# Optimization experiments

Hardware: AMD Instinct MI355X
Metric: run time of the kernel (lower is better)

Reference implementation:

```python
import jax, jax.numpy as jnp
import numpy as np

D_MODEL = 1024
DK = 64
N_HEADS = D_MODEL // DK
MASK = True


def setup_inputs() -> dict:
    key = jax.random.key(0)
    ks = jax.random.split(key, 8)
    B, S = 4, 2048
    scale = 1.0 / np.sqrt(D_MODEL)
    return {
        "query_data": jax.random.normal(ks[0], (B, S, D_MODEL), dtype=jnp.float32),
        "key_data": jax.random.normal(ks[1], (B, S, D_MODEL), dtype=jnp.float32),
        "value_data": jax.random.normal(ks[2], (B, S, D_MODEL), dtype=jnp.float32),
        "Wq": jax.random.normal(ks[3], (D_MODEL, D_MODEL), dtype=jnp.float32) * scale,
        "Wk": jax.random.normal(ks[4], (D_MODEL, D_MODEL), dtype=jnp.float32) * scale,
        "Wv": jax.random.normal(ks[5], (D_MODEL, D_MODEL), dtype=jnp.float32) * scale,
        "Wp": jax.random.normal(ks[6], (D_MODEL, D_MODEL), dtype=jnp.float32) * scale,
        "bp": jnp.zeros((D_MODEL,), dtype=jnp.float32),
    }


def reference(query_data, key_data, value_data, Wq, Wk, Wv, Wp, bp):
    B, S, _ = query_data.shape
    # QKV projections, split into heads: (B, H, S, dk)
    def split_heads(x, W):
        return (x @ W.T).reshape(B, -1, N_HEADS, DK).transpose(0, 2, 1, 3)

    q = split_heads(query_data, Wq)
    k = split_heads(key_data, Wk)
    v = split_heads(value_data, Wv)

    scores = jnp.einsum("bhqd,bhkd->bhqk", q, k) / np.sqrt(DK).astype(np.float32)
    if MASK:
        Sq, Sk = scores.shape[-2], scores.shape[-1]
        causal = jnp.triu(jnp.ones((Sq, Sk), dtype=scores.dtype), k=1) * jnp.float32(-1e13)
        scores = scores + causal  # broadcast over (B, H)
    attn = jax.nn.softmax(scores, axis=-1)
    out = jnp.einsum("bhqk,bhkd->bhqd", attn, v)
    out = out.transpose(0, 2, 1, 3).reshape(B, S, D_MODEL)
    # dropout is identity in eval mode
    return out @ Wp.T + bp
```

## Files before the change

### kernel.cpp

```cpp
#include <hip/hip_runtime.h>
#include <stdint.h>

#define D_MODEL 1024
#define SEQ     2048
#define BATCH   4
#define NH      16
#define DKK     64
#define MROWS   (BATCH * SEQ)

typedef unsigned short u16;
using bf16x8 = __attribute__((ext_vector_type(8))) __bf16;
using f32x4  = __attribute__((ext_vector_type(4))) float;

__device__ __forceinline__ u16 f2bf(float f) {
    union { float f; uint32_t u; } v; v.f = f;
    return (u16)((v.u + 0x7FFFu + ((v.u >> 16) & 1u)) >> 16);
}

__device__ __forceinline__ float fast_exp2(float x) {
    float r; asm("v_exp_f32 %0, %1" : "=v"(r) : "v"(x)); return r;
}
__device__ __forceinline__ float fast_rcp(float x) {
    float r; asm("v_rcp_f32 %0, %1" : "=v"(r) : "v"(x)); return r;
}

__device__ __forceinline__ void gl_lds16(const u16* g, u16* l) {
    __builtin_amdgcn_global_load_lds(
        (__attribute__((address_space(1))) void*)(const_cast<u16*>(g)),
        (__attribute__((address_space(3))) void*)l, 16, 0, 0);
}

__global__ __launch_bounds__(256) void cvt3_kernel(const float* __restrict__ a,
                                                   const float* __restrict__ b,
                                                   const float* __restrict__ c,
                                                   u16* __restrict__ da,
                                                   u16* __restrict__ db,
                                                   u16* __restrict__ dc) {
    const int i = blockIdx.x * 256 + threadIdx.x;
    const int sel = i >> 21, off = i & ((1 << 21) - 1);
    const float* s = (sel == 0) ? a : (sel == 1) ? b : c;
    u16* d = (sel == 0) ? da : (sel == 1) ? db : dc;
    float4 v = ((const float4*)s)[off];
    ushort4 o;
    o.x = f2bf(v.x); o.y = f2bf(v.y); o.z = f2bf(v.z); o.w = f2bf(v.w);
    ((ushort4*)d)[off] = o;
}

__global__ __launch_bounds__(256) void cvt4_kernel(const float* __restrict__ a,
                                                   const float* __restrict__ b,
                                                   const float* __restrict__ c,
                                                   const float* __restrict__ d4,
                                                   u16* __restrict__ da,
                                                   u16* __restrict__ db,
                                                   u16* __restrict__ dc,
                                                   u16* __restrict__ dd) {
    const int i = blockIdx.x * 256 + threadIdx.x;
    const int sel = i >> 18, off = i & ((1 << 18) - 1);
    const float* s = (sel == 0) ? a : (sel == 1) ? b : (sel == 2) ? c : d4;
    u16* d = (sel == 0) ? da : (sel == 1) ? db : (sel == 2) ? dc : dd;
    float4 v = ((const float4*)s)[off];
    ushort4 o;
    o.x = f2bf(v.x); o.y = f2bf(v.y); o.z = f2bf(v.z); o.w = f2bf(v.w);
    ((ushort4*)d)[off] = o;
}

__global__ __launch_bounds__(256, 2) void gemm_qkv(const u16* __restrict__ XQ,
                                                   const u16* __restrict__ XK,
                                                   const u16* __restrict__ XV,
                                                   const u16* __restrict__ WQ,
                                                   const u16* __restrict__ WK,
                                                   const u16* __restrict__ WV,
                                                   u16* __restrict__ Qo,
                                                   u16* __restrict__ Ko,
                                                   u16* __restrict__ Vto) {
    constexpr int K = 1024, N = 1024;
    __shared__ u16 ldsA[128 * 32];
    __shared__ u16 ldsB[128 * 32];

    const int which = blockIdx.x >> 9;
    const int inner = blockIdx.x & 511;
    const u16* A  = (which == 0) ? XQ : (which == 1) ? XK : XV;
    const u16* Bw = (which == 0) ? WQ : (which == 1) ? WK : WV;

    const int t = threadIdx.x;
    const int w = t >> 6, lane = t & 63;
    const int quad = lane >> 4, l15 = lane & 15;
    const int bn = inner & 7, bm = inner >> 3;
    const int wm = (w >> 1) * 64, wn = (w & 1) * 64;

    const u16* Ab = A  + (size_t)bm * 128 * K;
    const u16* Bb = Bw + (size_t)bn * 128 * K;
    const int srow  = lane >> 2;
    const int scol8 = (lane & 3) * 8;

    f32x4 acc[4][4];
    #pragma unroll
    for (int i = 0; i < 4; ++i)
        #pragma unroll
        for (int j = 0; j < 4; ++j)
            acc[i][j] = f32x4{0.f, 0.f, 0.f, 0.f};

    for (int k0 = 0; k0 < K; k0 += 32) {
        __syncthreads();
        #pragma unroll
        for (int i = 0; i < 2; ++i) {
            const int c = w * 2 + i;
            gl_lds16(Ab + (size_t)(c * 16 + srow) * K + k0 + scol8, &ldsA[c * 512]);
            gl_lds16(Bb + (size_t)(c * 16 + srow) * K + k0 + scol8, &ldsB[c * 512]);
        }
        __syncthreads();

        bf16x8 afr[4], bfr[4];
        #pragma unroll
        for (int i = 0; i < 4; ++i)
            afr[i] = *(const bf16x8*)&ldsA[(wm + i * 16 + l15) * 32 + quad * 8];
        #pragma unroll
        for (int j = 0; j < 4; ++j)
            bfr[j] = *(const bf16x8*)&ldsB[(wn + j * 16 + l15) * 32 + quad * 8];

        #pragma unroll
        for (int i = 0; i < 4; ++i)
            #pragma unroll
            for (int j = 0; j < 4; ++j)
                acc[i][j] = __builtin_amdgcn_mfma_f32_16x16x32_bf16(afr[i], bfr[j], acc[i][j], 0, 0, 0);
    }

    if (which < 2) {
        u16* outb = which ? Ko : Qo;
        #pragma unroll
        for (int i = 0; i < 4; ++i)
            #pragma unroll
            for (int j = 0; j < 4; ++j)
                #pragma unroll
                for (int r = 0; r < 4; ++r) {
                    const int row = bm * 128 + wm + i * 16 + quad * 4 + r;
                    const int col = bn * 128 + wn + j * 16 + l15;
                    outb[(size_t)row * N + col] = f2bf(acc[i][j][r]);
                }
    } else {
        #pragma unroll
        for (int i = 0; i < 4; ++i)
            #pragma unroll
            for (int j = 0; j < 4; ++j)
                #pragma unroll
                for (int r = 0; r < 4; ++r) {
                    const int row = bm * 128 + wm + i * 16 + quad * 4 + r;
                    const int col = bn * 128 + wn + j * 16 + l15;
                    const int bb = row >> 11, ss = row & 2047;
                    const int hh = col >> 6,  dd = col & 63;
                    Vto[(size_t)((bb * NH + hh) * DKK + dd) * SEQ + ss] = f2bf(acc[i][j][r]);
                }
    }
}

__global__ __launch_bounds__(256, 2) void gemm_proj(const u16* __restrict__ A,
                                                    const u16* __restrict__ Bw,
                                                    float* __restrict__ outf,
                                                    const float* __restrict__ bias) {
    constexpr int K = 1024, N = 1024;
    __shared__ u16 ldsA[128 * 32];
    __shared__ u16 ldsB[128 * 32];

    const int t = threadIdx.x;
    const int w = t >> 6, lane = t & 63;
    const int quad = lane >> 4, l15 = lane & 15;
    const int bn = blockIdx.x & 7, bm = blockIdx.x >> 3;
    const int wm = (w >> 1) * 64, wn = (w & 1) * 64;

    const u16* Ab = A  + (size_t)bm * 128 * K;
    const u16* Bb = Bw + (size_t)bn * 128 * K;
    const int srow  = lane >> 2;
    const int scol8 = (lane & 3) * 8;

    f32x4 acc[4][4];
    #pragma unroll
    for (int i = 0; i < 4; ++i)
        #pragma unroll
        for (int j = 0; j < 4; ++j)
            acc[i][j] = f32x4{0.f, 0.f, 0.f, 0.f};

    for (int k0 = 0; k0 < K; k0 += 32) {
        __syncthreads();
        #pragma unroll
        for (int i = 0; i < 2; ++i) {
            const int c = w * 2 + i;
            gl_lds16(Ab + (size_t)(c * 16 + srow) * K + k0 + scol8, &ldsA[c * 512]);
            gl_lds16(Bb + (size_t)(c * 16 + srow) * K + k0 + scol8, &ldsB[c * 512]);
        }
        __syncthreads();

        bf16x8 afr[4], bfr[4];
        #pragma unroll
        for (int i = 0; i < 4; ++i)
            afr[i] = *(const bf16x8*)&ldsA[(wm + i * 16 + l15) * 32 + quad * 8];
        #pragma unroll
        for (int j = 0; j < 4; ++j)
            bfr[j] = *(const bf16x8*)&ldsB[(wn + j * 16 + l15) * 32 + quad * 8];

        #pragma unroll
        for (int i = 0; i < 4; ++i)
            #pragma unroll
            for (int j = 0; j < 4; ++j)
                acc[i][j] = __builtin_amdgcn_mfma_f32_16x16x32_bf16(afr[i], bfr[j], acc[i][j], 0, 0, 0);
    }

    #pragma unroll
    for (int i = 0; i < 4; ++i)
        #pragma unroll
        for (int j = 0; j < 4; ++j)
            #pragma unroll
            for (int r = 0; r < 4; ++r) {
                const int row = bm * 128 + wm + i * 16 + quad * 4 + r;
                const int col = bn * 128 + wn + j * 16 + l15;
                outf[(size_t)row * N + col] = acc[i][j][r] + bias[col];
            }
}

__global__ __launch_bounds__(256, 4) void flash_attn(const u16* __restrict__ Qb,
                                                     const u16* __restrict__ Kb,
                                                     const u16* __restrict__ Vt,
                                                     u16* __restrict__ O) {
    __shared__ u16 ldsK[2 * 4096];
    __shared__ u16 ldsV[2 * 4096];
    __shared__ u16 ldsP[4 * 1024];

    const int t = threadIdx.x;
    const int w = t >> 6, lane = t & 63;
    const int quad = lane >> 4, l15 = lane & 15;
    const int bh = blockIdx.x & 63;
    const int qt = blockIdx.x >> 6;
    const int b = bh >> 4, h = bh & 15;
    const int q0 = qt * 64;
    const int qw = q0 + w * 16;

    const int srow  = lane >> 2;
    const int scol8 = (lane & 3) * 8;
    const size_t kbase = (size_t)b * SEQ * D_MODEL + h * DKK;
    const size_t vbase = (size_t)(bh * DKK) * SEQ;

    const u16* Qrow = Qb + (size_t)(b * SEQ + qw + l15) * D_MODEL + h * DKK;
    const bf16x8 qf0 = *(const bf16x8*)(Qrow + quad * 8);
    const bf16x8 qf1 = *(const bf16x8*)(Qrow + 32 + quad * 8);

    bf16x8 onesf;
    {
        union { bf16x8 v; u16 s[8]; } uu;
        const u16 ov = (l15 == 0) ? (u16)0x3F80 : (u16)0;
        #pragma unroll
        for (int j = 0; j < 8; ++j) uu.s[j] = ov;
        onesf = uu.v;
    }

    f32x4 o_acc[4];
    #pragma unroll
    for (int nt = 0; nt < 4; ++nt) o_acc[nt] = f32x4{0.f, 0.f, 0.f, 0.f};
    float m_i[4], l_i[4];
    #pragma unroll
    for (int r = 0; r < 4; ++r) { m_i[r] = -1e30f; l_i[r] = 0.f; }

    const float C2 = 0.18033688f;

    {
        #pragma unroll
        for (int i = 0; i < 2; ++i) {
            const int e = w * 2 + i, ch = e >> 2, rb = (e & 3) * 16;
            gl_lds16(Kb + kbase + (size_t)(0 + rb + srow) * D_MODEL + ch * 32 + scol8,
                     &ldsK[ch * 2048 + rb * 32]);
            gl_lds16(Vt + vbase + (size_t)(rb + srow) * SEQ + 0 + ch * 32 + scol8,
                     &ldsV[ch * 2048 + rb * 32]);
        }
    }

    int cur = 0;
    for (int it = 0; it <= qt; ++it) {
        const int kb = it * 64;
        __syncthreads();

        if (it < qt) {
            const int nb = (it + 1) * 64, nxt = cur ^ 1;
            #pragma unroll
            for (int i = 0; i < 2; ++i) {
                const int e = w * 2 + i, ch = e >> 2, rb = (e & 3) * 16;
                gl_lds16(Kb + kbase + (size_t)(nb + rb + srow) * D_MODEL + ch * 32 + scol8,
                         &ldsK[nxt * 4096 + ch * 2048 + rb * 32]);
                gl_lds16(Vt + vbase + (size_t)(rb + srow) * SEQ + nb + ch * 32 + scol8,
                         &ldsV[nxt * 4096 + ch * 2048 + rb * 32]);
            }
        }

        f32x4 sc[4];
        #pragma unroll
        for (int jt = 0; jt < 4; ++jt) sc[jt] = f32x4{0.f, 0.f, 0.f, 0.f};
        #pragma unroll
        for (int ks = 0; ks < 2; ++ks) {
            const bf16x8 qf = ks ? qf1 : qf0;
            #pragma unroll
            for (int jt = 0; jt < 4; ++jt) {
                bf16x8 kf = *(const bf16x8*)&ldsK[cur * 4096 + ks * 2048 + (jt * 16 + l15) * 32 + quad * 8];
                sc[jt] = __builtin_amdgcn_mfma_f32_16x16x32_bf16(qf, kf, sc[jt], 0, 0, 0);
            }
        }

        if (kb + 63 > qw) {
            #pragma unroll
            for (int jt = 0; jt < 4; ++jt)
                #pragma unroll
                for (int r = 0; r < 4; ++r)
                    if (kb + jt * 16 + l15 > qw + quad * 4 + r) sc[jt][r] = -3.0e38f;
        }

        float tmax[4];
        #pragma unroll
        for (int r = 0; r < 4; ++r)
            tmax[r] = fmaxf(fmaxf(sc[0][r], sc[1][r]), fmaxf(sc[2][r], sc[3][r]));
        #pragma unroll
        for (int off = 1; off < 16; off <<= 1)
            #pragma unroll
            for (int r = 0; r < 4; ++r)
                tmax[r] = fmaxf(tmax[r], __shfl_xor(tmax[r], off));

        float alpha[4];
        #pragma unroll
        for (int r = 0; r < 4; ++r) {
            const float mn = fmaxf(m_i[r], tmax[r] * C2);
            alpha[r] = fast_exp2(m_i[r] - mn);
            m_i[r] = mn;
        }

        #pragma unroll
        for (int jt = 0; jt < 4; ++jt) {
            const int g = (jt * 2 + (l15 >> 3)) ^ quad;
            #pragma unroll
            for (int r = 0; r < 4; ++r) {
                const float p = fast_exp2(fmaf(sc[jt][r], C2, -m_i[r]));
                ldsP[w * 1024 + (quad * 4 + r) * 64 + g * 8 + (l15 & 7)] = f2bf(p);
            }
        }

        #pragma unroll
        for (int nt = 0; nt < 4; ++nt)
            #pragma unroll
            for (int r = 0; r < 4; ++r)
                o_acc[nt][r] *= alpha[r];

        asm volatile("s_waitcnt lgkmcnt(0)" ::: "memory");

        f32x4 lacc = f32x4{0.f, 0.f, 0.f, 0.f};
        #pragma unroll
        for (int ks = 0; ks < 2; ++ks) {
            const int gg = (ks * 4 + quad) ^ (l15 >> 2);
            bf16x8 pf = *(const bf16x8*)&ldsP[w * 1024 + l15 * 64 + gg * 8];
            lacc = __builtin_amdgcn_mfma_f32_16x16x32_bf16(pf, onesf, lacc, 0, 0, 0);
            #pragma unroll
            for (int nt = 0; nt < 4; ++nt) {
                bf16x8 vf = *(const bf16x8*)&ldsV[cur * 4096 + ks * 2048 + (nt * 16 + l15) * 32 + quad * 8];
                o_acc[nt] = __builtin_amdgcn_mfma_f32_16x16x32_bf16(pf, vf, o_acc[nt], 0, 0, 0);
            }
        }

        #pragma unroll
        for (int r = 0; r < 4; ++r) {
            const float ts = __shfl(lacc[r], (lane & 48));
            l_i[r] = fmaf(l_i[r], alpha[r], ts);
        }

        cur ^= 1;
    }

    float rl[4];
    #pragma unroll
    for (int r = 0; r < 4; ++r) rl[r] = fast_rcp(l_i[r]);
    #pragma unroll
    for (int nt = 0; nt < 4; ++nt)
        #pragma unroll
        for (int r = 0; r < 4; ++r) {
            const int qg = qw + quad * 4 + r;
            O[(size_t)(b * SEQ + qg) * D_MODEL + h * DKK + nt * 16 + l15] = f2bf(o_acc[nt][r] * rl[r]);
        }
}

extern "C" void kernel_launch(void* const* d_in, const int* in_sizes, int n_in,
                              void* d_out, int out_size, void* d_ws, size_t ws_size,
                              hipStream_t stream) {
    const float* q_in = (const float*)d_in[0];
    const float* k_in = (const float*)d_in[1];
    const float* v_in = (const float*)d_in[2];
    const float* Wq   = (const float*)d_in[3];
    const float* Wk   = (const float*)d_in[4];
    const float* Wv   = (const float*)d_in[5];
    const float* Wp   = (const float*)d_in[6];
    const float* bp   = (const float*)d_in[7];
    float* out = (float*)d_out;

    char* ws = (char*)d_ws;
    u16* XQ  = (u16*)(ws + (size_t)0);
    u16* XK  = (u16*)(ws + ((size_t)16 << 20));
    u16* XV  = (u16*)(ws + ((size_t)32 << 20));
    u16* WQb = (u16*)(ws + ((size_t)48 << 20));
    u16* WKb = (u16*)(ws + ((size_t)50 << 20));
    u16* WVb = (u16*)(ws + ((size_t)52 << 20));
    u16* WPb = (u16*)(ws + ((size_t)54 << 20));
    u16* Qb  = (u16*)(ws + ((size_t)56 << 20));
    u16* Kb  = (u16*)(ws + ((size_t)72 << 20));
    u16* Vtb = (u16*)(ws + ((size_t)88 << 20));

    cvt3_kernel<<<3 * (1 << 21) / 256, 256, 0, stream>>>(q_in, k_in, v_in, XQ, XK, XV);
    cvt4_kernel<<<4 * (1 << 18) / 256, 256, 0, stream>>>(Wq, Wk, Wv, Wp, WQb, WKb, WVb, WPb);

    gemm_qkv<<<1536, 256, 0, stream>>>(XQ, XK, XV, WQb, WKb, WVb, Qb, Kb, Vtb);

    flash_attn<<<BATCH * NH * (SEQ / 64), 256, 0, stream>>>(Qb, Kb, Vtb, XQ);

    gemm_proj<<<512, 256, 0, stream>>>(XQ, WPb, out, bp);
}
```

Before: 372.7 us.

## Transpose scores layout in attention, stage V transpose via LDS, reverse tile order

The attention kernel now computes S^T (K as the A operand), so each lane owns one query row. That lets the row max and sum be done with two cross-lane shuffles, replaces the ones-vector MFMA row-sum, and writes P to LDS as packed 8-byte stores with an XOR swizzle. The QKV GEMM now stages the V output tile through a padded LDS buffer so the transposed V^T store becomes coalesced 16-byte writes instead of strided scalar stores. Query tiles are launched in reverse order so the longest causal blocks start first, which should improve load balance. It also adds LDS alignment attributes, extra shuffles to broadcast alpha and 1/l per row, and a larger shared allocation in gemm_qkv that may reduce occupancy.

```diff
diff --git a/kernel.cpp b/kernel.cpp
--- a/kernel.cpp
+++ b/kernel.cpp
@@ -74,8 +74,10 @@
                                                    u16* __restrict__ Ko,
                                                    u16* __restrict__ Vto) {
     constexpr int K = 1024, N = 1024;
-    __shared__ u16 ldsA[128 * 32];
-    __shared__ u16 ldsB[128 * 32];
+    __shared__ __align__(16) u16 smem[17408];
+    u16* ldsA = smem;
+    u16* ldsB = smem + 4096;
+    u16* ldsT = smem;
 
     const int which = blockIdx.x >> 9;
     const int inner = blockIdx.x & 511;
@@ -138,18 +140,28 @@
                     outb[(size_t)row * N + col] = f2bf(acc[i][j][r]);
                 }
     } else {
+        __syncthreads();
         #pragma unroll
         for (int i = 0; i < 4; ++i)
             #pragma unroll
             for (int j = 0; j < 4; ++j)
                 #pragma unroll
                 for (int r = 0; r < 4; ++r) {
-                    const int row = bm * 128 + wm + i * 16 + quad * 4 + r;
-                    const int col = bn * 128 + wn + j * 16 + l15;
-                    const int bb = row >> 11, ss = row & 2047;
-                    const int hh = col >> 6,  dd = col & 63;
-                    Vto[(size_t)((bb * NH + hh) * DKK + dd) * SEQ + ss] = f2bf(acc[i][j][r]);
+                    const int row_l = wm + i * 16 + quad * 4 + r;
+                    const int col_l = wn + j * 16 + l15;
+                    ldsT[col_l * 136 + row_l] = f2bf(acc[i][j][r]);
                 }
+        __syncthreads();
+        const int c = t >> 1, half = t & 1;
+        const int colg = bn * 128 + c;
+        const int hh = colg >> 6, dd = colg & 63;
+        const int bb = bm >> 4;
+        const int s0 = ((bm * 128) & 2047) + half * 64;
+        const u16* srcl = ldsT + c * 136 + half * 64;
+        u16* dstg = Vto + (size_t)((bb * NH + hh) * DKK + dd) * SEQ + s0;
+        #pragma unroll
+        for (int k = 0; k < 8; ++k)
+            *(uint4*)(dstg + k * 8) = *(const uint4*)(srcl + k * 8);
     }
 }
 
@@ -158,8 +170,8 @@
                                                     float* __restrict__ outf,
                                                     const float* __restrict__ bias) {
     constexpr int K = 1024, N = 1024;
-    __shared__ u16 ldsA[128 * 32];
-    __shared__ u16 ldsB[128 * 32];
+    __shared__ __align__(16) u16 ldsA[128 * 32];
+    __shared__ __align__(16) u16 ldsB[128 * 32];
 
     const int t = threadIdx.x;
     const int w = t >> 6, lane = t & 63;
@@ -220,15 +232,15 @@
                                                      const u16* __restrict__ Kb,
                                                      const u16* __restrict__ Vt,
                                                      u16* __restrict__ O) {
-    __shared__ u16 ldsK[2 * 4096];
-    __shared__ u16 ldsV[2 * 4096];
-    __shared__ u16 ldsP[4 * 1024];
+    __shared__ __align__(16) u16 ldsK[2 * 4096];
+    __shared__ __align__(16) u16 ldsV[2 * 4096];
+    __shared__ __align__(16) u16 ldsP[4 * 1024];
 
     const int t = threadIdx.x;
     const int w = t >> 6, lane = t & 63;
     const int quad = lane >> 4, l15 = lane & 15;
     const int bh = blockIdx.x & 63;
-    const int qt = blockIdx.x >> 6;
+    const int qt = 31 - (blockIdx.x >> 6);
     const int b = bh >> 4, h = bh & 15;
     const int q0 = qt * 64;
     const int qw = q0 + w * 16;
@@ -242,31 +254,22 @@
     const bf16x8 qf0 = *(const bf16x8*)(Qrow + quad * 8);
     const bf16x8 qf1 = *(const bf16x8*)(Qrow + 32 + quad * 8);
 
-    bf16x8 onesf;
-    {
-        union { bf16x8 v; u16 s[8]; } uu;
-        const u16 ov = (l15 == 0) ? (u16)0x3F80 : (u16)0;
-        #pragma unroll
-        for (int j = 0; j < 8; ++j) uu.s[j] = ov;
-        onesf = uu.v;
-    }
-
     f32x4 o_acc[4];
     #pragma unroll
     for (int nt = 0; nt < 4; ++nt) o_acc[nt] = f32x4{0.f, 0.f, 0.f, 0.f};
-    float m_i[4], l_i[4];
-    #pragma unroll
-    for (int r = 0; r < 4; ++r) { m_i[r] = -1e30f; l_i[r] = 0.f; }
+    float m_i = -1e30f, l_i = 0.f;
 
     const float C2 = 0.18033688f;
+
+    u16* PwS = &ldsP[w * 1024 + l15 * 64];
 
     {
         #pragma unroll
         for (int i = 0; i < 2; ++i) {
             const int e = w * 2 + i, ch = e >> 2, rb = (e & 3) * 16;
-            gl_lds16(Kb + kbase + (size_t)(0 + rb + srow) * D_MODEL + ch * 32 + scol8,
+            gl_lds16(Kb + kbase + (size_t)(rb + srow) * D_MODEL + ch * 32 + scol8,
                      &ldsK[ch * 2048 + rb * 32]);
-            gl_lds16(Vt + vbase + (size_t)(rb + srow) * SEQ + 0 + ch * 32 + scol8,
+            gl_lds16(Vt + vbase + (size_t)(rb + srow) * SEQ + ch * 32 + scol8,
                      &ldsV[ch * 2048 + rb * 32]);
         }
     }
@@ -297,7 +300,7 @@
             #pragma unroll
             for (int jt = 0; jt < 4; ++jt) {
                 bf16x8 kf = *(const bf16x8*)&ldsK[cur * 4096 + ks * 2048 + (jt * 16 + l15) * 32 + quad * 8];
-                sc[jt] = __builtin_amdgcn_mfma_f32_16x16x32_bf16(qf, kf, sc[jt], 0, 0, 0);
+                sc[jt] = __builtin_amdgcn_mfma_f32_16x16x32_bf16(kf, qf, sc[jt], 0, 0, 0);
             }
         }
 
@@ -306,70 +309,74 @@
             for (int jt = 0; jt < 4; ++jt)
                 #pragma unroll
                 for (int r = 0; r < 4; ++r)
-                    if (kb + jt * 16 + l15 > qw + quad * 4 + r) sc[jt][r] = -3.0e38f;
-        }
-
-        float tmax[4];
+                    if (kb + jt * 16 + quad * 4 + r > qw + l15) sc[jt][r] = -3.0e38f;
+        }
+
+        float tmax = sc[0][0];
+        #pragma unroll
+        for (int jt = 0; jt < 4; ++jt)
+            #pragma unroll
+            for (int r = 0; r < 4; ++r) tmax = fmaxf(tmax, sc[jt][r]);
+        tmax = fmaxf(tmax, __shfl_xor(tmax, 16));
+        tmax = fmaxf(tmax, __shfl_xor(tmax, 32));
+
+        const float mn = fmaxf(m_i, tmax * C2);
+        const float alpha = fast_exp2(m_i - mn);
+        m_i = mn;
+
+        float tsum = 0.f;
+        #pragma unroll
+        for (int jt = 0; jt < 4; ++jt) {
+            float p[4];
+            #pragma unroll
+            for (int r = 0; r < 4; ++r) {
+                p[r] = fast_exp2(fmaf(sc[jt][r], C2, -mn));
+                tsum += p[r];
+            }
+            const int pos = (4 * jt + quad) ^ l15;
+            uint2 pk;
+            pk.x = (uint32_t)f2bf(p[0]) | ((uint32_t)f2bf(p[1]) << 16);
+            pk.y = (uint32_t)f2bf(p[2]) | ((uint32_t)f2bf(p[3]) << 16);
+            *(uint2*)&PwS[pos * 4] = pk;
+        }
+        tsum += __shfl_xor(tsum, 16);
+        tsum += __shfl_xor(tsum, 32);
+        l_i = fmaf(l_i, alpha, tsum);
+
+        float al[4];
         #pragma unroll
         for (int r = 0; r < 4; ++r)
-            tmax[r] = fmaxf(fmaxf(sc[0][r], sc[1][r]), fmaxf(sc[2][r], sc[3][r]));
-        #pragma unroll
-        for (int off = 1; off < 16; off <<= 1)
+            al[r] = __shfl(alpha, (lane & 48) | (quad * 4 + r));
+        #pragma unroll
+        for (int nt = 0; nt < 4; ++nt)
             #pragma unroll
             for (int r = 0; r < 4; ++r)
-                tmax[r] = fmaxf(tmax[r], __shfl_xor(tmax[r], off));
-
-        float alpha[4];
-        #pragma unroll
-        for (int r = 0; r < 4; ++r) {
-            const float mn = fmaxf(m_i[r], tmax[r] * C2);
-            alpha[r] = fast_exp2(m_i[r] - mn);
-            m_i[r] = mn;
-        }
-
-        #pragma unroll
-        for (int jt = 0; jt < 4; ++jt) {
-            const int g = (jt * 2 + (l15 >> 3)) ^ quad;
-            #pragma unroll
-            for (int r = 0; r < 4; ++r) {
-                const float p = fast_exp2(fmaf(sc[jt][r], C2, -m_i[r]));
-                ldsP[w * 1024 + (quad * 4 + r) * 64 + g * 8 + (l15 & 7)] = f2bf(p);
-            }
-        }
-
-        #pragma unroll
-        for (int nt = 0; nt < 4; ++nt)
-            #pragma unroll
-            for (int r = 0; r < 4; ++r)
-                o_acc[nt][r] *= alpha[r];
+                o_acc[nt][r] *= al[r];
 
         asm volatile("s_waitcnt lgkmcnt(0)" ::: "memory");
 
-        f32x4 lacc = f32x4{0.f, 0.f, 0.f, 0.f};
         #pragma unroll
         for (int ks = 0; ks < 2; ++ks) {
-            const int gg = (ks * 4 + quad) ^ (l15 >> 2);
-            bf16x8 pf = *(const bf16x8*)&ldsP[w * 1024 + l15 * 64 + gg * 8];
-            lacc = __builtin_amdgcn_mfma_f32_16x16x32_bf16(pf, onesf, lacc, 0, 0, 0);
+            const int g = 8 * ks + 2 * quad;
+            uint2 lo = *(const uint2*)&PwS[((g    ) ^ l15) * 4];
+            uint2 hi = *(const uint2*)&PwS[((g + 1) ^ l15) * 4];
+            union { bf16x8 v; uint2 u[2]; } pu;
+            pu.u[0] = lo; pu.u[1] = hi;
             #pragma unroll
             for (int nt = 0; nt < 4; ++nt) {
                 bf16x8 vf = *(const bf16x8*)&ldsV[cur * 4096 + ks * 2048 + (nt * 16 + l15) * 32 + quad * 8];
-                o_acc[nt] = __builtin_amdgcn_mfma_f32_16x16x32_bf16(pf, vf, o_acc[nt], 0, 0, 0);
+                o_acc[nt] = __builtin_amdgcn_mfma_f32_16x16x32_bf16(pu.v, vf, o_acc[nt], 0, 0, 0);
             }
-        }
-
-        #pragma unroll
-        for (int r = 0; r < 4; ++r) {
-            const float ts = __shfl(lacc[r], (lane & 48));
-            l_i[r] = fmaf(l_i[r], alpha[r], ts);
         }
 
         cur ^= 1;
     }
 
+    const float rli = fast_rcp(l_i);
     float rl[4];
     #pragma unroll
-    for (int r = 0; r < 4; ++r) rl[r] = fast_rcp(l_i[r]);
+    for (int r = 0; r < 4; ++r)
+        rl[r] = __shfl(rli, (lane & 48) | (quad * 4 + r));
     #pragma unroll
     for (int nt = 0; nt < 4; ++nt)
         #pragma unroll
```

New measurement: 347.8 us. 1.07x faster.
